# Kernel optimization log

Measured on AMD Instinct MI355X. Metric: run time of the kernel, lower is better.

Reference implementation:

```python
import jax, jax.numpy as jnp
import numpy as np
import math

N, DS, DV, R, B = 65536, 256, 64, 64, 8
H = DV  # GVP hidden vector channels = max(vi, vo)
EPS = 1e-8
SCALE = 1.0 / math.sqrt(DS + 3 * DV)  # d_total = scalar_dim + 3*vector_dim


def _gvp(s, v, wh, ws_w, ws_b, wv, wsv_w, wsv_b):
    # full GVP with vector_gate=True, activations=(silu, sigmoid)
    vt = jnp.swapaxes(v, -1, -2)                                  # [N, 3, DV]
    vh = vt @ wh.T                                                # [N, 3, H]
    vn = jnp.sqrt(jnp.clip(jnp.sum(vh * vh, axis=-2), EPS))       # [N, H] norm_no_nan
    s_out = jnp.concatenate([s, vn], axis=-1) @ ws_w.T + ws_b     # [N, DS]
    v_out = jnp.swapaxes(vh @ wv.T, -1, -2)                       # [N, DV, 3]
    gate = jax.nn.sigmoid(s_out) @ wsv_w.T + wsv_b                # vector_act(s) then wsv
    v_out = v_out * jax.nn.sigmoid(gate)[..., None]
    return jax.nn.silu(s_out), v_out


def _gvp_scalar(s, v, wh, ws_w, ws_b):
    # gate_gvp: vo=0, activations=(None, None) -> scalar output only
    vt = jnp.swapaxes(v, -1, -2)
    vh = vt @ wh.T
    vn = jnp.sqrt(jnp.clip(jnp.sum(vh * vh, axis=-2), EPS))
    return jnp.concatenate([s, vn], axis=-1) @ ws_w.T + ws_b


def _layernorm(x, g, b):
    mu = x.mean(-1, keepdims=True)
    var = ((x - mu) ** 2).mean(-1, keepdims=True)
    return (x - mu) / jnp.sqrt(var + 1e-5) * g + b


def setup_inputs() -> dict:
    key = jax.random.key(0)
    ks = jax.random.split(key, 32)

    def lin(k, fo, fi):
        return (jax.random.normal(k, (fo, fi), jnp.float32) / np.sqrt(fi)).astype(jnp.float32)

    inp = {
        'x_s': jax.random.normal(ks[0], (N, DS), jnp.float32),
        'x_v': jax.random.normal(ks[1], (N, DV, 3), jnp.float32),
        'batch_index': jnp.sort(jax.random.randint(ks[2], (N,), 0, B, jnp.int32)),
    }
    i = 3
    for name in ('q', 'k', 'v', 'o'):
        inp[f'{name}_wh'] = lin(ks[i], H, DV)
        inp[f'{name}_ws_w'] = lin(ks[i + 1], DS, DS + H)
        inp[f'{name}_ws_b'] = jnp.zeros((DS,), jnp.float32)
        inp[f'{name}_wv'] = lin(ks[i + 2], DV, H)
        inp[f'{name}_wsv_w'] = lin(ks[i + 3], DV, DS)
        inp[f'{name}_wsv_b'] = jnp.zeros((DV,), jnp.float32)
        i += 4
    inp['comp_w1'] = lin(ks[i], DS, DS)
    inp['comp_b1'] = jnp.zeros((DS,), jnp.float32)
    inp['ln_g'] = jnp.ones((DS,), jnp.float32)
    inp['ln_b'] = jnp.zeros((DS,), jnp.float32)
    inp['comp_w2'] = lin(ks[i + 1], R, DS)
    inp['comp_b2'] = jnp.zeros((R,), jnp.float32)
    inp['g_wh'] = lin(ks[i + 2], H, DV)
    inp['g_ws_w'] = lin(ks[i + 3], DS, DS + H)
    inp['g_ws_b'] = jnp.zeros((DS,), jnp.float32)
    inp['gate_bias'] = jnp.full((DS,), -1.0, jnp.float32)
    return inp


def reference(x_s, x_v, batch_index,
              q_wh, q_ws_w, q_ws_b, q_wv, q_wsv_w, q_wsv_b,
              k_wh, k_ws_w, k_ws_b, k_wv, k_wsv_w, k_wsv_b,
              v_wh, v_ws_w, v_ws_b, v_wv, v_wsv_w, v_wsv_b,
              o_wh, o_ws_w, o_ws_b, o_wv, o_wsv_w, o_wsv_b,
              comp_w1, comp_b1, ln_g, ln_b, comp_w2, comp_b2,
              g_wh, g_ws_w, g_ws_b, gate_bias):
    Q_s, Q_v = _gvp(x_s, x_v, q_wh, q_ws_w, q_ws_b, q_wv, q_wsv_w, q_wsv_b)
    K_s, K_v = _gvp(x_s, x_v, k_wh, k_ws_w, k_ws_b, k_wv, k_wsv_w, k_wsv_b)
    V_s, V_v = _gvp(x_s, x_v, v_wh, v_ws_w, v_ws_b, v_wv, v_wsv_w, v_wsv_b)

    h = _layernorm(x_s @ comp_w1.T + comp_b1, ln_g, ln_b)
    P = jax.nn.softmax(jax.nn.silu(h) @ comp_w2.T + comp_b2, axis=-1)  # [N, R]

    out_s = jnp.zeros_like(x_s)
    out_v = jnp.zeros_like(x_v)
    # per-graph anchor compression + retrieval (B is a small fixed graph count)
    for b in range(B):
        m = (batch_index == b).astype(x_s.dtype)                  # [N]
        Pm = P * m[:, None]                                       # masked soft assignment
        Kbs = Pm.T @ K_s                                          # [R, DS]
        Vbs = Pm.T @ V_s                                          # [R, DS]
        Kbv = jnp.einsum('nr,nvc->rvc', Pm, K_v)                  # [R, DV, 3]
        Vbv = jnp.einsum('nr,nvc->rvc', Pm, V_v)                  # [R, DV, 3]
        logits = (Q_s @ Kbs.T + jnp.einsum('nvc,rvc->nr', Q_v, Kbv)) * SCALE
        attn = jax.nn.softmax(logits, axis=-1)                    # [N, R]
        out_s = out_s + m[:, None] * (attn @ Vbs)
        out_v = out_v + m[:, None, None] * jnp.einsum('nr,rvc->nvc', attn, Vbv)

    gate_s = jax.nn.sigmoid(_gvp_scalar(x_s, x_v, g_wh, g_ws_w, g_ws_b) + gate_bias)
    gate_v = jax.nn.sigmoid(gate_s.mean(-1, keepdims=True))[..., None]
    return _gvp(out_s * gate_s, out_v * gate_v,
                o_wh, o_ws_w, o_ws_b, o_wv, o_wsv_w, o_wsv_b)
```

## Files before the change

### kernel.cpp

```cpp
#include <hip/hip_runtime.h>

typedef unsigned short u16;
typedef __attribute__((ext_vector_type(8))) short bs8;
typedef __attribute__((ext_vector_type(4))) short bs4;
typedef __attribute__((ext_vector_type(4))) float fx4;
#define MFMA16(a,b,c) __builtin_amdgcn_mfma_f32_16x16x32_bf16(a,b,c,0,0,0)

__device__ __forceinline__ float b2f(u16 u){ return __uint_as_float(((unsigned int)u) << 16); }
__device__ __forceinline__ u16 f2b(float f){
  unsigned int x = __float_as_uint(f);
  unsigned int r = (x + 0x7FFFu + ((x >> 16) & 1u)) >> 16;
  return (u16)r;
}
__device__ __forceinline__ float rcpf(float x){ return __builtin_amdgcn_rcpf(x); }
__device__ __forceinline__ float sigm(float x){ return rcpf(1.f+__expf(-x)); }
__device__ __forceinline__ float siluf(float x){ return x*rcpf(1.f+__expf(-x)); }
__device__ __forceinline__ float wsum(float v){
  #pragma unroll
  for (int o=1;o<64;o<<=1) v += __shfl_xor(v, o);
  return v;
}
__device__ __forceinline__ float wmax(float v){
  #pragma unroll
  for (int o=1;o<64;o<<=1) v = fmaxf(v, __shfl_xor(v, o));
  return v;
}
__device__ __forceinline__ bs8 lds8(const u16* ptr){ return *reinterpret_cast<const bs8*>(ptr); }
__device__ __forceinline__ bs8 glb8(const u16* ptr){ return *reinterpret_cast<const bs8*>(ptr); }

#define XSB_P 328
#define XVB_P 72
#define SGB_P 264
#define UBUF_P 68
#define XQ_P 456
#define AT_P 72

struct GP {
  const float* x_s; const float* x_v; const int* bidx;
  const float* wh[5]; const float* ws_w[5]; const float* ws_b[5];
  const float* wv[4]; const float* wsv_w[4]; const float* wsv_b[4];
  const float *w1, *b1, *lng, *lnb, *w2, *b2, *gbias;
  u16 *wsP, *whP, *wvP, *wsvP, *w1P, *w2P;
  float *wsb_f, *wsvb_f, *b1_f, *b2_f, *lng_f, *lnb_f, *gb_f;
  u16 *KP, *VP, *Gs, *PT, *QB;
  float *Gv, *CK, *CV;
  u16 *CKP, *CVP;
  int *bstart;
  float *Qs, *Qv;
};

__global__ __launch_bounds__(256) void kprep(GP p){
  int idx = blockIdx.x*256 + threadIdx.x;
  if (idx < 409600){
    int s=idx/81920, r=idx%81920;
    int ks=r/8192, r2=r%8192, nt=r2/512, r3=r2%512, ln=r3/8, j=r3%8;
    int n=nt*16+(ln&15), k=ks*32+((ln>>4)*8)+j;
    p.wsP[idx] = f2b(p.ws_w[s][n*320+k]); return;
  }
  idx -= 409600;
  if (idx < 20480){
    int s=idx/4096, r=idx%4096;
    int ks=r/2048, r2=r%2048, nt=r2/512, r3=r2%512, ln=r3/8, j=r3%8;
    int h=nt*16+(ln&15), d=ks*32+((ln>>4)*8)+j;
    p.whP[idx] = f2b(p.wh[s][h*64+d]); return;
  }
  idx -= 20480;
  if (idx < 16384){
    int s=idx/4096, r=idx%4096;
    int ks=r/2048, r2=r%2048, nt=r2/512, r3=r2%512, ln=r3/8, j=r3%8;
    int dd=nt*16+(ln&15), hh=ks*32+((ln>>4)*8)+j;
    p.wvP[idx] = f2b(p.wv[s][dd*64+hh]); return;
  }
  idx -= 16384;
  if (idx < 65536){
    int s=idx/16384, r=idx%16384;
    int ks=r/2048, r2=r%2048, nt=r2/512, r3=r2%512, ln=r3/8, j=r3%8;
    int dd=nt*16+(ln&15), i=ks*32+((ln>>4)*8)+j;
    p.wsvP[idx] = f2b(p.wsv_w[s][dd*256+i]); return;
  }
  idx -= 65536;
  if (idx < 65536){
    int ks=idx/8192, r2=idx%8192, nt=r2/512, r3=r2%512, ln=r3/8, j=r3%8;
    int n=nt*16+(ln&15), k=ks*32+((ln>>4)*8)+j;
    p.w1P[idx] = f2b(p.w1[n*256+k]); return;
  }
  idx -= 65536;
  if (idx < 16384){
    int ks=idx/2048, r2=idx%2048, nt=r2/512, r3=r2%512, ln=r3/8, j=r3%8;
    int rr=nt*16+(ln&15), i=ks*32+((ln>>4)*8)+j;
    p.w2P[idx] = f2b(p.w2[rr*256+i]); return;
  }
  idx -= 16384;
  if (idx < 1280){ int s=idx>>8, i=idx&255; p.wsb_f[idx] = p.ws_b[s][i]; return; }
  idx -= 1280;
  if (idx < 256){ int s=idx>>6, d=idx&63; p.wsvb_f[idx] = p.wsv_b[s][d]; return; }
  idx -= 256;
  if (idx < 256){ p.b1_f[idx] = p.b1[idx]; return; }
  idx -= 256;
  if (idx < 64){ p.b2_f[idx] = p.b2[idx]; return; }
  idx -= 64;
  if (idx < 256){ p.lng_f[idx] = p.lng[idx]; return; }
  idx -= 256;
  if (idx < 256){ p.lnb_f[idx] = p.lnb[idx]; return; }
  idx -= 256;
  if (idx < 256){ p.gb_f[idx] = p.gbias[idx]; return; }
  idx -= 256;
  if (idx < 65536){
    if (idx == 0){
      int b0 = p.bidx[0];
      for (int b=0;b<=b0;b++) p.bstart[b]=0;
      int bl = p.bidx[65535];
      for (int b=bl+1;b<=8;b++) p.bstart[b]=65536;
    } else {
      int a = p.bidx[idx-1], c = p.bidx[idx];
      for (int b=a+1;b<=c;b++) p.bstart[b] = idx;
    }
    return;
  }
}

__device__ __forceinline__ void mfma_vh_vn(const u16* whPs, const u16* xvb, u16* vhb2,
                                           u16* xsb, int lane, int w4){
  fx4 a0={0,0,0,0}, a1={0,0,0,0}, a2={0,0,0,0};
  #pragma unroll
  for (int ks=0; ks<2; ks++){
    bs8 b = glb8(whPs + (ks*4+w4)*512 + lane*8);
    bs8 x0 = lds8(xvb + ( 0 + (lane&15))*XVB_P + ks*32 + ((lane>>4)*8));
    bs8 x1 = lds8(xvb + (16 + (lane&15))*XVB_P + ks*32 + ((lane>>4)*8));
    bs8 x2 = lds8(xvb + (32 + (lane&15))*XVB_P + ks*32 + ((lane>>4)*8));
    a0 = MFMA16(x0,b,a0); a1 = MFMA16(x1,b,a1); a2 = MFMA16(x2,b,a2);
  }
  int h = w4*16 + (lane&15);
  int mrow = (lane>>4)*4;
  #pragma unroll
  for (int r=0;r<4;r++){
    vhb2[( 0+mrow+r)*XVB_P + h] = f2b(a0[r]);
    vhb2[(16+mrow+r)*XVB_P + h] = f2b(a1[r]);
    vhb2[(32+mrow+r)*XVB_P + h] = f2b(a2[r]);
    float nv = __builtin_amdgcn_sqrtf(
        fmaxf(a0[r]*a0[r] + a1[r]*a1[r] + a2[r]*a2[r], 1e-8f));
    xsb[(mrow+r)*XSB_P + 256 + h] = f2b(nv);
  }
  __syncthreads();
}

template<int KS>
__device__ __forceinline__ void mfma_sgemm2(const u16* wsPs, const float* bias,
                                            const u16* xsb, int lane, int wave,
                                            fx4 acc[2][2]){
  #pragma unroll
  for (int h=0;h<2;h++)
    #pragma unroll
    for (int t=0;t<2;t++) acc[h][t]=(fx4){0.f,0.f,0.f,0.f};
  const u16* arow0 = xsb + (lane&15)*XSB_P + ((lane>>4)*8);
  const u16* arow1 = arow0 + 16*XSB_P;
  #pragma unroll
  for (int ks=0; ks<KS; ks++){
    bs8 a0 = lds8(arow0 + ks*32);
    bs8 a1 = lds8(arow1 + ks*32);
    bs8 b0 = glb8(wsPs + (ks*16 + wave*2+0)*512 + lane*8);
    bs8 b1 = glb8(wsPs + (ks*16 + wave*2+1)*512 + lane*8);
    acc[0][0]=MFMA16(a0,b0,acc[0][0]); acc[0][1]=MFMA16(a0,b1,acc[0][1]);
    acc[1][0]=MFMA16(a1,b0,acc[1][0]); acc[1][1]=MFMA16(a1,b1,acc[1][1]);
  }
  #pragma unroll
  for (int t=0;t<2;t++){
    float bv = bias[(wave*2+t)*16 + (lane&15)];
    #pragma unroll
    for (int h=0;h<2;h++){
      acc[h][t][0]+=bv; acc[h][t][1]+=bv; acc[h][t][2]+=bv; acc[h][t][3]+=bv;
    }
  }
}

__device__ __forceinline__ fx4 mfma_g64(const u16* bP, const u16* sgb, int lane, int w4){
  fx4 acc = {0.f,0.f,0.f,0.f};
  const u16* arow = sgb + (lane&15)*SGB_P + ((lane>>4)*8);
  #pragma unroll
  for (int ks=0; ks<8; ks++){
    bs8 a = lds8(arow + ks*32);
    bs8 b = glb8(bP + (ks*4 + w4)*512 + lane*8);
    acc = MFMA16(a,b,acc);
  }
  return acc;
}

__device__ __forceinline__ void mfma_wv(const u16* wvPs, const u16* vhb2,
                                        int lane, int w4, fx4 vo[3]){
  vo[0]=(fx4){0.f,0.f,0.f,0.f}; vo[1]=vo[0]; vo[2]=vo[0];
  #pragma unroll
  for (int ks=0; ks<2; ks++){
    bs8 b = glb8(wvPs + (ks*4+w4)*512 + lane*8);
    #pragma unroll
    for (int c=0;c<3;c++){
      bs8 a = lds8(vhb2 + (c*16 + (lane&15))*XVB_P + ks*32 + ((lane>>4)*8));
      vo[c] = MFMA16(a,b,vo[c]);
    }
  }
}

__global__ __launch_bounds__(512, 4) void k1(GP p){
  __shared__ __align__(16) u16 xsb[32*XSB_P];
  __shared__ __align__(16) u16 xvb[96*XVB_P];
  __shared__ __align__(16) u16 vhb2[96*XVB_P];
  __shared__ __align__(16) u16 sgb[32*SGB_P];
  __shared__ float red[2][8][16];
  __shared__ float redb[2][8][16];
  __shared__ float lnp[2][2][16];
  __shared__ float ubuf[32*UBUF_P];
  const int tid = threadIdx.x, lane = tid&63, wave = tid>>6;
  const int w4 = wave&3, hv = wave>>2;
  const int ml = lane&15, gl = lane>>4;
  const int n0 = blockIdx.x * 32;
  u16* xsbH  = xsb  + hv*16*XSB_P;
  u16* xvbH  = xvb  + hv*48*XVB_P;
  u16* vhb2H = vhb2 + hv*48*XVB_P;
  u16* sgbH  = sgb  + hv*16*SGB_P;

  for (int i=tid;i<2048;i+=512){
    int node=i>>6, c4=(i&63)*4;
    float4 v = *reinterpret_cast<const float4*>(p.x_s + (size_t)(n0+node)*256 + c4);
    u16* d = xsb + node*XSB_P + c4;
    d[0]=f2b(v.x); d[1]=f2b(v.y); d[2]=f2b(v.z); d[3]=f2b(v.w);
  }
  for (int i=tid;i<6144;i+=512){
    int row=i>>6, d=i&63;
    int h=row/48, rr=row-48*h, c=rr>>4, nl=rr&15;
    xvb[row*XVB_P+d] = f2b(p.x_v[(size_t)(n0+h*16+nl)*192 + d*3 + c]);
  }
  __syncthreads();

  fx4 acc[2][2];
  #pragma unroll 1
  for (int s=0; s<3; ++s){
    mfma_vh_vn(p.whP + s*4096, xvbH, vhb2H, xsbH, lane, w4);
    mfma_sgemm2<10>(p.wsP + (size_t)s*81920, p.wsb_f + s*256, xsb, lane, wave, acc);
    bs4 stv[2][2];
    #pragma unroll
    for (int h=0;h<2;h++){
      #pragma unroll
      for (int t=0;t<2;t++){
        int ncol=(wave*2+t)*16+ml;
        #pragma unroll
        for (int r=0;r<4;r++){
          int node16=gl*4+r;
          float v=acc[h][t][r];
          float sg=rcpf(1.f+__expf(-v));
          stv[h][t][r]=(short)f2b(v*sg);
          sgb[(h*16+node16)*SGB_P+ncol]=f2b(sg);
        }
      }
    }
    __syncthreads();
    if (s==0){
      #pragma unroll
      for (int h=0;h<2;h++)
        #pragma unroll
        for (int t=0;t<2;t++){
          int ncol=(wave*2+t)*16+ml;
          #pragma unroll
          for (int r=0;r<4;r++)
            p.QB[(size_t)(n0+h*16+gl*4+r)*448+ncol]=(u16)stv[h][t][r];
        }
    } else {
      u16* KVp = (s==1)? p.KP : p.VP;
      #pragma unroll
      for (int h=0;h<2;h++)
        #pragma unroll
        for (int t=0;t<2;t++){
          int ncol=(wave*2+t)*16+ml;
          *reinterpret_cast<bs4*>(KVp + ((size_t)((n0>>4)+h)*448 + ncol)*16 + gl*4) = stv[h][t];
        }
    }
    fx4 g = mfma_g64(p.wsvP + s*16384, sgbH, lane, w4);
    fx4 vo[3];
    mfma_wv(p.wvP + s*4096, vhb2H, lane, w4, vo);
    int dout = w4*16+ml;
    const int nb = n0 + hv*16;
    if (s==0){
      #pragma unroll
      for (int r=0;r<4;r++){
        int node=gl*4+r;
        float gg = sigm(g[r] + p.wsvb_f[dout]);
        #pragma unroll
        for (int c=0;c<3;c++)
          p.QB[(size_t)(nb+node)*448 + 256 + c*64 + dout] = f2b(vo[c][r]*gg);
      }
    } else {
      u16* KVp=(s==1)?p.KP:p.VP;
      float gg[4];
      #pragma unroll
      for (int r=0;r<4;r++) gg[r] = sigm(g[r] + p.wsvb_f[s*64+dout]);
      #pragma unroll
      for (int c=0;c<3;c++){
        bs4 st;
        #pragma unroll
        for (int r=0;r<4;r++) st[r]=(short)f2b(vo[c][r]*gg[r]);
        *reinterpret_cast<bs4*>(KVp + ((size_t)((n0>>4)+hv)*448 + 256 + c*64 + dout)*16 + gl*4) = st;
      }
    }
    __syncthreads();
  }

  mfma_vh_vn(p.whP + 3*4096, xvbH, vhb2H, xsbH, lane, w4);
  mfma_sgemm2<10>(p.wsP + (size_t)3*81920, p.wsb_f + 3*256, xsb, lane, wave, acc);
  {
    float psum[2][4] = {{0.f,0.f,0.f,0.f},{0.f,0.f,0.f,0.f}};
    u16 gsv[2][2][4];
    #pragma unroll
    for (int h=0;h<2;h++){
      #pragma unroll
      for (int t=0;t<2;t++){
        int ncol=(wave*2+t)*16+ml;
        float gb = p.gb_f[ncol];
        #pragma unroll
        for (int r=0;r<4;r++){
          float gs = sigm(acc[h][t][r] + gb);
          gsv[h][t][r]=f2b(gs);
          psum[h][r] += gs;
        }
      }
    }
    #pragma unroll
    for (int h=0;h<2;h++)
      #pragma unroll
      for (int r=0;r<4;r++){
        #pragma unroll
        for (int o=1;o<16;o<<=1) psum[h][r] += __shfl_xor(psum[h][r], o);
      }
    if (ml==0){
      #pragma unroll
      for (int h=0;h<2;h++)
        #pragma unroll
        for (int r=0;r<4;r++) red[h][wave][gl*4+r] = psum[h][r];
    }
    __syncthreads();
    #pragma unroll
    for (int h=0;h<2;h++)
      #pragma unroll
      for (int t=0;t<2;t++){
        int ncol=(wave*2+t)*16+ml;
        #pragma unroll
        for (int r=0;r<4;r++)
          p.Gs[(size_t)(n0+h*16+gl*4+r)*256+ncol] = gsv[h][t][r];
      }
    if (tid<32){
      int h=tid>>4, nl=tid&15;
      float s8 = red[h][0][nl]+red[h][1][nl]+red[h][2][nl]+red[h][3][nl]
               + red[h][4][nl]+red[h][5][nl]+red[h][6][nl]+red[h][7][nl];
      p.Gv[n0+tid] = sigm(s8*(1.f/256.f));
    }
    __syncthreads();
  }

  mfma_sgemm2<8>(p.w1P, p.b1_f, xsb, lane, wave, acc);
  {
    float s1[2][4]={{0.f,0.f,0.f,0.f},{0.f,0.f,0.f,0.f}};
    float s2[2][4]={{0.f,0.f,0.f,0.f},{0.f,0.f,0.f,0.f}};
    #pragma unroll
    for (int h=0;h<2;h++)
      #pragma unroll
      for (int t=0;t<2;t++)
        #pragma unroll
        for (int r=0;r<4;r++){ float v=acc[h][t][r]; s1[h][r]+=v; s2[h][r]+=v*v; }
    #pragma unroll
    for (int h=0;h<2;h++)
      #pragma unroll
      for (int r=0;r<4;r++){
        #pragma unroll
        for (int o=1;o<16;o<<=1){ s1[h][r]+=__shfl_xor(s1[h][r],o); s2[h][r]+=__shfl_xor(s2[h][r],o); }
      }
    if (ml==0){
      #pragma unroll
      for (int h=0;h<2;h++)
        #pragma unroll
        for (int r=0;r<4;r++){
          red[h][wave][gl*4+r]=s1[h][r];
          redb[h][wave][gl*4+r]=s2[h][r];
        }
    }
    __syncthreads();
    if (tid<32){
      int h=tid>>4, nl=tid&15;
      float S1=red[h][0][nl]+red[h][1][nl]+red[h][2][nl]+red[h][3][nl]
             + red[h][4][nl]+red[h][5][nl]+red[h][6][nl]+red[h][7][nl];
      float S2=redb[h][0][nl]+redb[h][1][nl]+redb[h][2][nl]+redb[h][3][nl]
             + redb[h][4][nl]+redb[h][5][nl]+redb[h][6][nl]+redb[h][7][nl];
      float mu=S1*(1.f/256.f), var=S2*(1.f/256.f)-mu*mu;
      lnp[h][0][nl]=mu; lnp[h][1][nl]=rsqrtf(var+1e-5f);
    }
    __syncthreads();
    #pragma unroll
    for (int h=0;h<2;h++)
      #pragma unroll
      for (int t=0;t<2;t++){
        int ncol=(wave*2+t)*16+ml;
        float g=p.lng_f[ncol], b=p.lnb_f[ncol];
        #pragma unroll
        for (int r=0;r<4;r++){
          int node16=gl*4+r;
          float hh=(acc[h][t][r]-lnp[h][0][node16])*lnp[h][1][node16]*g + b;
          sgb[(h*16+node16)*SGB_P+ncol]=f2b(siluf(hh));
        }
      }
    __syncthreads();
    fx4 u = mfma_g64(p.w2P, sgbH, lane, w4);
    int rcol = w4*16+ml;
    float b2v = p.b2_f[rcol];
    #pragma unroll
    for (int r=0;r<4;r++)
      ubuf[(hv*16 + gl*4+r)*UBUF_P + rcol] = u[r] + b2v;
    __syncthreads();
    bs4 pt4;
    #pragma unroll
    for (int i=0;i<4;i++){
      int node = wave*4+i;
      float uu = ubuf[node*UBUF_P + lane];
      float m = wmax(uu);
      float e = __expf(uu-m);
      float ss = wsum(e);
      pt4[i] = (short)f2b(e*rcpf(ss));
    }
    *reinterpret_cast<bs4*>(p.PT + ((size_t)((n0>>4)+(wave>>2))*64 + lane)*16 + (wave&3)*4) = pt4;
  }
}

__device__ __forceinline__ bs8 ldfrag(const u16* base, int n8, int row, int stride){
  return *reinterpret_cast<const bs8*>(base + ((size_t)(n8>>4)*stride + row)*16 + (n8&15));
}

__global__ __launch_bounds__(256) void k2(GP p){
  const int bid = blockIdx.x;
  const int bb = bid >> 5;
  const int sv = (bid >> 4) & 1;
  const int sp = bid & 15;
  const int lane = threadIdx.x & 63, wave = threadIdx.x >> 6;
  const int ml = lane & 15, gl = lane >> 4;
  int s0 = p.bstart[bb], s1 = p.bstart[bb+1];
  int len = s1 - s0; if (len <= 0) return;
  int cl = (((len + 15) >> 4) + 7) & ~7;
  int kb0 = s0 + sp*cl; if (kb0 >= s1) return;
  int kb1 = kb0 + cl; if (kb1 > s1) kb1 = s1;
  int kba = kb0 & ~7;
  const u16* F = sv ? p.VP : p.KP;
  fx4 acc[4][7];
  #pragma unroll
  for (int m=0;m<4;m++)
    #pragma unroll
    for (int t=0;t<7;t++) acc[m][t]=(fx4){0.f,0.f,0.f,0.f};

  for (int kb = kba; kb < kb1; kb += 32){
    int n8 = kb + gl*8;
    bool edge = (kb < kb0) | (kb + 32 > kb1);
    bs8 a[4];
    #pragma unroll
    for (int m=0;m<4;m++) a[m] = ldfrag(p.PT, n8, m*16+ml, 64);
    if (edge){
      #pragma unroll
      for (int j=0;j<8;j++){
        int n = n8 + j;
        if (n < kb0 || n >= kb1){
          #pragma unroll
          for (int m=0;m<4;m++) a[m][j]=0;
        }
      }
    }
    #pragma unroll
    for (int t=0;t<7;t++){
      bs8 bf = ldfrag(F, n8, (wave*7+t)*16+ml, 448);
      if (edge){
        #pragma unroll
        for (int j=0;j<8;j++){
          int n = n8 + j;
          if (n < kb0 || n >= kb1) bf[j]=0;
        }
      }
      #pragma unroll
      for (int m=0;m<4;m++) acc[m][t] = MFMA16(a[m], bf, acc[m][t]);
    }
  }
  #pragma unroll
  for (int m=0;m<4;m++){
    #pragma unroll
    for (int t=0;t<7;t++){
      int f = (wave*7+t)*16 + ml;
      int r0 = m*16 + gl*4;
      if (sv==0){
        float* dst = p.CK + ((size_t)bb*448+f)*64 + r0;
        #pragma unroll
        for (int j=0;j<4;j++) atomicAdd(dst+j, acc[m][t][j]);
      } else {
        float* dst = p.CV + ((size_t)bb*64+r0)*448 + f;
        #pragma unroll
        for (int j=0;j<4;j++) atomicAdd(dst + (size_t)j*448, acc[m][t][j]);
      }
    }
  }
}

__global__ __launch_bounds__(256) void k2b(GP p){
  int idx = blockIdx.x*256 + threadIdx.x;
  if (idx < 229376){
    int b=idx/28672, r=idx%28672;
    int ks=r/2048, r2=r%2048, nt=r2/512, r3=r2%512, ln=r3/8, j=r3&7;
    int f=ks*32+((ln>>4)*8)+j, rr=nt*16+(ln&15);
    p.CKP[idx] = f2b(p.CK[((size_t)b*448+f)*64+rr] * 0.047245559f);
    return;
  }
  idx -= 229376;
  int b=idx/28672, r=idx%28672;
  int ks=r/14336, r2=r%14336, nt=r2/512, r3=r2%512, ln=r3/8, j=r3&7;
  int rr=ks*32+((ln>>4)*8)+j, f=nt*16+(ln&15);
  p.CVP[idx] = f2b(p.CV[((size_t)b*64+rr)*448+f]);
}

__global__ __launch_bounds__(512, 4) void k3(GP p){
  __shared__ __align__(16) char smem[68608];
  u16* xq   = (u16*)smem;
  u16* atb  = (u16*)(smem+29184);
  u16* xsb  = (u16*)(smem+33792);
  u16* xvb  = (u16*)(smem+54784);
  u16* vhb2 = (u16*)smem;
  u16* sgb  = (u16*)(smem+13824);
  __shared__ float redm[2][4][16];
  __shared__ float reds[2][4][16];
  __shared__ int Bl[32];
  const int tid = threadIdx.x;
  const int n0 = blockIdx.x * 32;
  const int lane = tid & 63, wave = tid >> 6;
  const int w4 = wave&3, hv = wave>>2;
  const int ml = lane&15, gl = lane>>4;
  const int nb = n0 + hv*16;
  u16* xqH   = xq   + hv*16*XQ_P;
  u16* atbH  = atb  + hv*16*AT_P;
  u16* xsbH  = xsb  + hv*16*XSB_P;
  u16* xvbH  = xvb  + hv*48*XVB_P;
  u16* vhb2H = vhb2 + hv*48*XVB_P;
  u16* sgbH  = sgb  + hv*16*SGB_P;
  const int* BlH = Bl + hv*16;

  for (int idx=tid; idx<1792; idx+=512){
    int node = idx/56, q = idx-node*56;
    bs8 v = *reinterpret_cast<const bs8*>(p.QB + (size_t)(n0+node)*448 + q*8);
    *reinterpret_cast<bs8*>(xq + node*XQ_P + q*8) = v;
  }
  if (tid<32) Bl[tid] = p.bidx[n0+tid];
  __syncthreads();

  int bb = Bl[0];
  while (true){
    fx4 lac = {0.f,0.f,0.f,0.f};
    {
      const u16* ckb = p.CKP + (size_t)bb*28672;
      const u16* arow = xqH + ml*XQ_P + gl*8;
      #pragma unroll
      for (int ks=0; ks<14; ks++){
        bs8 a = lds8(arow + ks*32);
        bs8 b = glb8(ckb + (ks*4+w4)*512 + lane*8);
        lac = MFMA16(a,b,lac);
      }
    }
    float loc[4];
    #pragma unroll
    for (int r=0;r<4;r++){
      float m = lac[r];
      #pragma unroll
      for (int o=1;o<16;o<<=1) m = fmaxf(m, __shfl_xor(m,o));
      loc[r]=m;
    }
    if (ml==0){
      #pragma unroll
      for (int r=0;r<4;r++) redm[hv][w4][gl*4+r]=loc[r];
    }
    __syncthreads();
    float e4[4];
    #pragma unroll
    for (int r=0;r<4;r++){
      int node=gl*4+r;
      float gm = fmaxf(fmaxf(redm[hv][0][node],redm[hv][1][node]),
                       fmaxf(redm[hv][2][node],redm[hv][3][node]));
      float e = __expf(lac[r]-gm);
      e4[r]=e;
      float s=e;
      #pragma unroll
      for (int o=1;o<16;o<<=1) s += __shfl_xor(s,o);
      loc[r]=s;
    }
    if (ml==0){
      #pragma unroll
      for (int r=0;r<4;r++) reds[hv][w4][gl*4+r]=loc[r];
    }
    __syncthreads();
    #pragma unroll
    for (int r=0;r<4;r++){
      int node=gl*4+r;
      float tot = reds[hv][0][node]+reds[hv][1][node]+reds[hv][2][node]+reds[hv][3][node];
      atbH[node*AT_P + w4*16 + ml] = f2b(e4[r]*rcpf(tot));
    }
    __syncthreads();
    {
      const u16* cvb = p.CVP + (size_t)bb*28672;
      const u16* prow = atbH + ml*AT_P + gl*8;
      bs8 a0 = lds8(prow);
      bs8 a1 = lds8(prow + 32);
      #pragma unroll
      for (int t=0;t<7;t++){
        int nt = w4*7 + t;
        fx4 pv = {0.f,0.f,0.f,0.f};
        pv = MFMA16(a0, glb8(cvb + nt*512 + lane*8), pv);
        pv = MFMA16(a1, glb8(cvb + (28+nt)*512 + lane*8), pv);
        int f = nt*16 + ml;
        #pragma unroll
        for (int r=0;r<4;r++){
          int node=gl*4+r;
          if (BlH[node]!=bb) continue;
          int n = nb+node;
          if (f < 256){
            float gs = b2f(p.Gs[(size_t)n*256+f]);
            xsbH[node*XSB_P+f] = f2b(pv[r]*gs);
          } else {
            int fm=f-256, c=fm>>6, d=fm&63;
            xvbH[(c*16+node)*XVB_P+d] = f2b(pv[r]*p.Gv[n]);
          }
        }
      }
    }
    int nxt = 0x7fffffff;
    #pragma unroll
    for (int i=0;i<32;i++){ int v=Bl[i]; if (v>bb && v<nxt) nxt=v; }
    if (nxt==0x7fffffff) break;
    bb = nxt;
    __syncthreads();
  }
  __syncthreads();

  mfma_vh_vn(p.whP + 4*4096, xvbH, vhb2H, xsbH, lane, w4);
  fx4 acc[2][2];
  mfma_sgemm2<10>(p.wsP + (size_t)4*81920, p.wsb_f + 4*256, xsb, lane, wave, acc);
  #pragma unroll
  for (int h=0;h<2;h++){
    #pragma unroll
    for (int t=0;t<2;t++){
      int ncol=(wave*2+t)*16+ml;
      #pragma unroll
      for (int r=0;r<4;r++){
        int node16=gl*4+r;
        float v=acc[h][t][r];
        float sg=rcpf(1.f+__expf(-v));
        p.Qs[(size_t)(n0+h*16+node16)*256+ncol]=v*sg;
        sgb[(h*16+node16)*SGB_P+ncol]=f2b(sg);
      }
    }
  }
  __syncthreads();
  fx4 g = mfma_g64(p.wsvP + 3*16384, sgbH, lane, w4);
  fx4 vo[3];
  mfma_wv(p.wvP + 3*4096, vhb2H, lane, w4, vo);
  int dout = w4*16+ml;
  #pragma unroll
  for (int r=0;r<4;r++){
    int node=gl*4+r;
    float gg = sigm(g[r] + p.wsvb_f[3*64+dout]);
    #pragma unroll
    for (int c=0;c<3;c++)
      p.Qv[(size_t)(nb+node)*192 + dout*3 + c] = vo[c][r]*gg;
  }
}

extern "C" void kernel_launch(void* const* d_in, const int* in_sizes, int n_in,
                              void* d_out, int out_size, void* d_ws, size_t ws_size,
                              hipStream_t stream){
  (void)in_sizes; (void)n_in; (void)out_size; (void)ws_size;
  GP p;
  p.x_s  = (const float*)d_in[0];
  p.x_v  = (const float*)d_in[1];
  p.bidx = (const int*)d_in[2];
  const int whI[5]  = {3, 9, 15, 33, 21};
  const int wswI[5] = {4, 10, 16, 34, 22};
  const int wsbI[5] = {5, 11, 17, 35, 23};
  const int wvI[4]  = {6, 12, 18, 24};
  const int wsvwI[4]= {7, 13, 19, 25};
  const int wsvbI[4]= {8, 14, 20, 26};
  for (int s=0;s<5;s++){
    p.wh[s]   = (const float*)d_in[whI[s]];
    p.ws_w[s] = (const float*)d_in[wswI[s]];
    p.ws_b[s] = (const float*)d_in[wsbI[s]];
  }
  for (int s=0;s<4;s++){
    p.wv[s]    = (const float*)d_in[wvI[s]];
    p.wsv_w[s] = (const float*)d_in[wsvwI[s]];
    p.wsv_b[s] = (const float*)d_in[wsvbI[s]];
  }
  p.w1    = (const float*)d_in[27];
  p.b1    = (const float*)d_in[28];
  p.lng   = (const float*)d_in[29];
  p.lnb   = (const float*)d_in[30];
  p.w2    = (const float*)d_in[31];
  p.b2    = (const float*)d_in[32];
  p.gbias = (const float*)d_in[36];

  char* w = (char*)d_ws;
  auto alloc = [&](size_t bytes)->char*{
    char* r = w; w += (bytes + 255) & ~(size_t)255; return r;
  };
  p.wsP   = (u16*)alloc(409600u*2);
  p.whP   = (u16*)alloc(20480u*2);
  p.wvP   = (u16*)alloc(16384u*2);
  p.wsvP  = (u16*)alloc(65536u*2);
  p.w1P   = (u16*)alloc(65536u*2);
  p.w2P   = (u16*)alloc(16384u*2);
  p.wsb_f  = (float*)alloc(1280u*4);
  p.wsvb_f = (float*)alloc(256u*4);
  p.b1_f   = (float*)alloc(256u*4);
  p.b2_f   = (float*)alloc(64u*4);
  p.lng_f  = (float*)alloc(256u*4);
  p.lnb_f  = (float*)alloc(256u*4);
  p.gb_f   = (float*)alloc(256u*4);
  p.QB = (u16*)alloc((size_t)65536*448*2);
  p.KP = (u16*)alloc((size_t)65536*448*2 + (1u<<22));
  p.VP = (u16*)alloc((size_t)65536*448*2 + (1u<<22));
  p.Gs = (u16*)alloc((size_t)65536*256*2);
  p.PT = (u16*)alloc((size_t)65536*64*2 + (1u<<20));
  p.Gv = (float*)alloc((size_t)65536*4);
  p.CK = (float*)alloc((size_t)8*448*64*4);
  p.CV = (float*)alloc((size_t)8*448*64*4);
  p.CKP = (u16*)alloc((size_t)8*448*64*2);
  p.CVP = (u16*)alloc((size_t)8*448*64*2);
  p.bstart = (int*)alloc(64);
  p.Qs = (float*)d_out;
  p.Qv = (float*)d_out + (size_t)65536*256;

  hipMemsetAsync(p.CK, 0, (size_t)8*448*64*4, stream);
  hipMemsetAsync(p.CV, 0, (size_t)8*448*64*4, stream);
  kprep<<<2587, 256, 0, stream>>>(p);
  k1<<<2048, 512, 0, stream>>>(p);
  k2<<<256, 256, 0, stream>>>(p);
  k2b<<<1792, 256, 0, stream>>>(p);
  k3<<<2048, 512, 0, stream>>>(p);
}
```

Baseline: 725.8 us.

## Double k2 split count and apply gates in a vectorized post-pass

```diff
diff --git a/kernel.cpp b/kernel.cpp
--- a/kernel.cpp
+++ b/kernel.cpp
@@ -431,14 +431,14 @@
 
 __global__ __launch_bounds__(256) void k2(GP p){
   const int bid = blockIdx.x;
-  const int bb = bid >> 5;
-  const int sv = (bid >> 4) & 1;
-  const int sp = bid & 15;
+  const int bb = bid >> 6;
+  const int sv = (bid >> 5) & 1;
+  const int sp = bid & 31;
   const int lane = threadIdx.x & 63, wave = threadIdx.x >> 6;
   const int ml = lane & 15, gl = lane >> 4;
   int s0 = p.bstart[bb], s1 = p.bstart[bb+1];
   int len = s1 - s0; if (len <= 0) return;
-  int cl = (((len + 15) >> 4) + 7) & ~7;
+  int cl = (((len + 31) >> 5) + 7) & ~7;
   int kb0 = s0 + sp*cl; if (kb0 >= s1) return;
   int kb1 = kb0 + cl; if (kb1 > s1) kb1 = s1;
   int kba = kb0 & ~7;
@@ -614,13 +614,11 @@
         for (int r=0;r<4;r++){
           int node=gl*4+r;
           if (BlH[node]!=bb) continue;
-          int n = nb+node;
           if (f < 256){
-            float gs = b2f(p.Gs[(size_t)n*256+f]);
-            xsbH[node*XSB_P+f] = f2b(pv[r]*gs);
+            xsbH[node*XSB_P+f] = f2b(pv[r]);
           } else {
             int fm=f-256, c=fm>>6, d=fm&63;
-            xvbH[(c*16+node)*XVB_P+d] = f2b(pv[r]*p.Gv[n]);
+            xvbH[(c*16+node)*XVB_P+d] = f2b(pv[r]);
           }
         }
       }
@@ -631,6 +629,32 @@
     if (nxt==0x7fffffff) break;
     bb = nxt;
     __syncthreads();
+  }
+  __syncthreads();
+
+  for (int i=tid; i<1024; i+=512){
+    int node=i>>5, f8=(i&31)*8;
+    bs8 g8 = *reinterpret_cast<const bs8*>(p.Gs + (size_t)(n0+node)*256 + f8);
+    u16* xp = xsb + node*XSB_P + f8;
+    bs8 x8 = *reinterpret_cast<bs8*>(xp);
+    bs8 o8;
+    #pragma unroll
+    for (int j=0;j<8;j++)
+      o8[j] = (short)f2b(b2f((u16)x8[j]) * b2f((u16)g8[j]));
+    *reinterpret_cast<bs8*>(xp) = o8;
+  }
+  for (int i=tid; i<768; i+=512){
+    int node=i/24, g=i-node*24;
+    int fm=g*8, c=fm>>6, d=fm&63;
+    int row=(node>>4)*48 + c*16 + (node&15);
+    float gv = p.Gv[n0+node];
+    u16* xp = xvb + row*XVB_P + d;
+    bs8 x8 = *reinterpret_cast<bs8*>(xp);
+    bs8 o8;
+    #pragma unroll
+    for (int j=0;j<8;j++)
+      o8[j] = (short)f2b(b2f((u16)x8[j]) * gv);
+    *reinterpret_cast<bs8*>(xp) = o8;
   }
   __syncthreads();
 
@@ -734,7 +758,7 @@
   hipMemsetAsync(p.CV, 0, (size_t)8*448*64*4, stream);
   kprep<<<2587, 256, 0, stream>>>(p);
   k1<<<2048, 512, 0, stream>>>(p);
-  k2<<<256, 256, 0, stream>>>(p);
+  k2<<<512, 256, 0, stream>>>(p);
   k2b<<<1792, 256, 0, stream>>>(p);
   k3<<<2048, 512, 0, stream>>>(p);
 }
```

Result: faster. 687.0 us (-5.3%).
